# Kernel optimization log

Measured on AMD Instinct MI355X. Metric: run time of the kernel, lower is better.

## Reference

```python
import jax, jax.numpy as jnp
from jax import lax
import numpy as np


def _lap(cost):
    """Jonker-Volgenant shortest-augmenting-path LAP (same optimum as
    scipy.optimize.linear_sum_assignment) on cost [n, m] with n <= m.
    Returns for each row (0..n-1) the assigned column index."""
    n, m = cost.shape
    BIG = jnp.asarray(1e9, cost.dtype)
    a = jnp.pad(cost, ((1, 0), (1, 0)))  # 1-based rows/cols, [n+1, m+1]
    u = jnp.zeros(n + 1, cost.dtype)     # row duals
    v = jnp.zeros(m + 1, cost.dtype)     # col duals
    p = jnp.zeros(m + 1, jnp.int32)      # p[j] = row matched to col j (0 = free)

    def row_step(i, carry):
        u, v, p = carry
        p = p.at[0].set(i)  # virtual col 0 holds the row being inserted
        minv = jnp.full(m + 1, BIG, cost.dtype)
        used = jnp.zeros(m + 1, bool)
        way = jnp.zeros(m + 1, jnp.int32)

        def cond(s):
            u, v, p, way, minv, used, j0 = s
            return p[j0] != 0

        def body(s):
            u, v, p, way, minv, used, j0 = s
            used = used.at[j0].set(True)
            i0 = p[j0]
            cur = a[i0] - u[i0] - v                      # reduced costs, len m+1
            better = (cur < minv) & jnp.logical_not(used)
            minv = jnp.where(better, cur, minv)
            way = jnp.where(better, j0, way)
            masked = jnp.where(used, BIG, minv)
            j1 = jnp.argmin(masked).astype(jnp.int32)
            delta = masked[j1]
            u = u.at[p].add(jnp.where(used, delta, jnp.zeros((), cost.dtype)))
            v = jnp.where(used, v - delta, v)
            minv = jnp.where(used, minv, minv - delta)
            return (u, v, p, way, minv, used, j1)

        u, v, p, way, minv, used, j0 = lax.while_loop(
            cond, body, (u, v, p, way, minv, used, jnp.int32(0)))

        # backtrack the augmenting path
        def cond2(s):
            return s[1] != 0

        def body2(s):
            p, j0 = s
            j1 = way[j0]
            return (p.at[j0].set(p[j1]), j1)

        p, _ = lax.while_loop(cond2, body2, (p, j0))
        return (u, v, p)

    u, v, p = lax.fori_loop(1, n + 1, row_step, (u, v, p))
    # invert: row r (1-based) matched to col j  ->  ans[r-1] = j-1
    cols = jnp.arange(m + 1)
    valid = (p > 0) & (cols > 0)
    idx = jnp.where(valid, p - 1, n)  # invalid entries dumped into scratch slot n
    ans = jnp.zeros(n + 1, jnp.int32).at[idx].set((cols - 1).astype(jnp.int32))
    return ans[:n]


def _cdist_mm(x, y):
    """Batched euclidean cdist via the GEMM trick (torch use_mm_for_euclid_dist)."""
    x2 = jnp.sum(x * x, axis=-1)[..., :, None]   # [B, N, 1]
    y2 = jnp.sum(y * y, axis=-1)[..., None, :]   # [B, 1, M]
    xy = jnp.einsum('bnd,bmd->bnm', x, y)        # [B, N, M]
    return jnp.sqrt(jnp.maximum(x2 + y2 - 2.0 * xy, 0.0))


def setup_inputs() -> dict:
    key = jax.random.key(0)
    k1, k2 = jax.random.split(key)
    outputs = jax.random.normal(k1, (32, 512, 768), dtype=jnp.float32)
    targets = jax.random.normal(k2, (32, 200, 768), dtype=jnp.float32)
    return {"outputs": outputs, "targets": targets}


def reference(outputs, targets):
    # cost[b, n, m] = ||outputs[b, n] - targets[b, m]||_2  (block-diagonal slices
    # of the original cross-batch cdist are all that the matcher consumes)
    cost = _cdist_mm(outputs, targets)                       # [B, N, M]
    # solve with targets as rows (n=M <= m=N): pred column per gt row
    gt_to_pred = jax.vmap(_lap)(jnp.swapaxes(cost, 1, 2))    # [B, M]
    # scipy returns pred indices sorted ascending; replicate that ordering
    order = jnp.argsort(gt_to_pred, axis=1)                  # gt indices (index_j)
    index_i = jnp.take_along_axis(gt_to_pred, order, axis=1)
    index_j = order.astype(jnp.int32)
    return jnp.stack([index_i, index_j], axis=1)             # [B, 2, M] int32
```

## Files before the change

### kernel.cpp

```cpp
#include <hip/hip_runtime.h>
#include <math.h>

static constexpr int BATCH = 32;
static constexpr int NPRED = 512;
static constexpr int NTGT  = 200;
static constexpr int DIM   = 768;
#define BIGF 1e9f
#define INFF __builtin_inff()

__global__ __launch_bounds__(64) void row_norms_kernel(const float* __restrict__ x,
                                                       float* __restrict__ out) {
    int row = blockIdx.x;
    const float4* r = (const float4*)(x + (size_t)row * DIM);
    float s = 0.f;
#pragma unroll
    for (int k = 0; k < 3; ++k) {
        float4 v = r[threadIdx.x + 64 * k];
        s += v.x * v.x + v.y * v.y + v.z * v.z + v.w * v.w;
    }
#pragma unroll
    for (int off = 32; off; off >>= 1) s += __shfl_down(s, off);
    if (threadIdx.x == 0) out[row] = s;
}

__global__ __launch_bounds__(256) void cost_kernel(const float* __restrict__ O,
                                                   const float* __restrict__ T,
                                                   const float* __restrict__ no_arr,
                                                   const float* __restrict__ nt_arr,
                                                   float* __restrict__ cost) {
    const int b  = blockIdx.z;
    const int m0 = blockIdx.y * 64;
    const int n0 = blockIdx.x * 64;
    const float* Tb = T + (size_t)b * NTGT * DIM;
    const float* Ob = O + (size_t)b * NPRED * DIM;

    __shared__ __align__(16) float As[32][68];
    __shared__ __align__(16) float Bs[32][68];

    const int tid = threadIdx.x;
    const int tx = tid & 15;
    const int ty = tid >> 4;

    float acc[4][4] = {};

    for (int k0 = 0; k0 < DIM; k0 += 32) {
#pragma unroll
        for (int q = 0; q < 2; ++q) {
            int f = tid + q * 256;
            int r = f >> 3;
            int kk = (f & 7) << 2;
            int gm = m0 + r; if (gm > NTGT - 1) gm = NTGT - 1;
            float4 vA = *(const float4*)(Tb + (size_t)gm * DIM + k0 + kk);
            As[kk + 0][r] = vA.x; As[kk + 1][r] = vA.y;
            As[kk + 2][r] = vA.z; As[kk + 3][r] = vA.w;
            float4 vB = *(const float4*)(Ob + (size_t)(n0 + r) * DIM + k0 + kk);
            Bs[kk + 0][r] = vB.x; Bs[kk + 1][r] = vB.y;
            Bs[kk + 2][r] = vB.z; Bs[kk + 3][r] = vB.w;
        }
        __syncthreads();
#pragma unroll
        for (int k = 0; k < 32; ++k) {
            float4 a  = *(const float4*)&As[k][ty << 2];
            float4 bv = *(const float4*)&Bs[k][tx << 2];
            acc[0][0] += a.x * bv.x; acc[0][1] += a.x * bv.y;
            acc[0][2] += a.x * bv.z; acc[0][3] += a.x * bv.w;
            acc[1][0] += a.y * bv.x; acc[1][1] += a.y * bv.y;
            acc[1][2] += a.y * bv.z; acc[1][3] += a.y * bv.w;
            acc[2][0] += a.z * bv.x; acc[2][1] += a.z * bv.y;
            acc[2][2] += a.z * bv.z; acc[2][3] += a.z * bv.w;
            acc[3][0] += a.w * bv.x; acc[3][1] += a.w * bv.y;
            acc[3][2] += a.w * bv.z; acc[3][3] += a.w * bv.w;
        }
        __syncthreads();
    }

    {
        float4 nov = *(const float4*)(no_arr + b * NPRED + n0 + (tx << 2));
#pragma unroll
        for (int i = 0; i < 4; ++i) {
            int gm = m0 + (ty << 2) + i;
            if (gm < NTGT) {
                float ntv = nt_arr[b * NTGT + gm];
                float4 o;
                o.x = sqrtf(fmaxf(ntv + nov.x - 2.0f * acc[i][0], 0.0f));
                o.y = sqrtf(fmaxf(ntv + nov.y - 2.0f * acc[i][1], 0.0f));
                o.z = sqrtf(fmaxf(ntv + nov.z - 2.0f * acc[i][2], 0.0f));
                o.w = sqrtf(fmaxf(ntv + nov.w - 2.0f * acc[i][3], 0.0f));
                *(float4*)&cost[((size_t)b * NTGT + gm) * NPRED + n0 + (tx << 2)] = o;
            }
        }
    }
}

__device__ __forceinline__ int rl(int v, int l) {
    return __builtin_amdgcn_readlane(v, l);
}
__device__ __forceinline__ float rlf(float v, int l) {
    return __int_as_float(__builtin_amdgcn_readlane(__float_as_int(v), l));
}
__device__ __forceinline__ int sel8i(const int* a, int s) {
    int r = a[0];
#pragma unroll
    for (int k = 1; k < 8; ++k) r = (s == k) ? a[k] : r;
    return r;
}
__device__ __forceinline__ float sel8f(const float* a, int s) {
    float r = a[0];
#pragma unroll
    for (int k = 1; k < 8; ++k) r = (s == k) ? a[k] : r;
    return r;
}
__device__ __forceinline__ float dpp_min_f32(float x) {
    float t;
    t = __int_as_float(__builtin_amdgcn_update_dpp(__float_as_int(x), __float_as_int(x), 0x111, 0xF, 0xF, false)); x = fminf(x, t);
    t = __int_as_float(__builtin_amdgcn_update_dpp(__float_as_int(x), __float_as_int(x), 0x112, 0xF, 0xF, false)); x = fminf(x, t);
    t = __int_as_float(__builtin_amdgcn_update_dpp(__float_as_int(x), __float_as_int(x), 0x114, 0xF, 0xF, false)); x = fminf(x, t);
    t = __int_as_float(__builtin_amdgcn_update_dpp(__float_as_int(x), __float_as_int(x), 0x118, 0xF, 0xF, false)); x = fminf(x, t);
    t = __int_as_float(__builtin_amdgcn_update_dpp(__float_as_int(x), __float_as_int(x), 0x142, 0xF, 0xF, false)); x = fminf(x, t);
    t = __int_as_float(__builtin_amdgcn_update_dpp(__float_as_int(x), __float_as_int(x), 0x143, 0xF, 0xF, false)); x = fminf(x, t);
    return x;
}
__device__ __forceinline__ float tree8(const float* m, int& lq) {
    float v01 = (m[0] <= m[1]) ? m[0] : m[1];
    int   q01 = (m[0] <= m[1]) ? 0 : 1;
    float v23 = (m[2] <= m[3]) ? m[2] : m[3];
    int   q23 = (m[2] <= m[3]) ? 2 : 3;
    float v45 = (m[4] <= m[5]) ? m[4] : m[5];
    int   q45 = (m[4] <= m[5]) ? 4 : 5;
    float v67 = (m[6] <= m[7]) ? m[6] : m[7];
    int   q67 = (m[6] <= m[7]) ? 6 : 7;
    float v03 = (v01 <= v23) ? v01 : v23;
    int   q03 = (v01 <= v23) ? q01 : q23;
    float v47 = (v45 <= v67) ? v45 : v67;
    int   q47 = (v45 <= v67) ? q45 : q67;
    lq = (v03 <= v47) ? q03 : q47;
    return (v03 <= v47) ? v03 : v47;
}

__global__ __launch_bounds__(64) void lap_kernel(const float* __restrict__ cost,
                                                 int* __restrict__ out) {
    const int b = blockIdx.x;
    const int lane = threadIdx.x;
    const float* C = cost + (size_t)b * NTGT * NPRED;
    const float* Cl = C + lane * 8;

    __shared__ float u0[NTGT + 1];
    __shared__ int g2p[NTGT];

    for (int k = lane; k < NTGT + 1; k += 64) u0[k] = 0.f;

    float v[8], minv[8], up[8];
    int p_arr[8], way_arr[8];
#pragma unroll
    for (int q = 0; q < 8; ++q) {
        v[q] = 0.f; up[q] = 0.f; p_arr[q] = 0; way_arr[q] = 0;
    }
    __syncthreads();

    float4 ca = *(const float4*)(Cl);
    float4 cb = *(const float4*)(Cl + 4);
    float4 sa = ca, sb = cb;

    for (int i = 1; i <= NTGT; ++i) {
#pragma unroll
        for (int q = 0; q < 8; ++q) minv[q] = BIGF;
        float uI = 0.f;
        float u_i0 = 0.f;
        int j0 = 0;
        int j1 = 0;
        int spec_j = 0;

        for (int it = 0; it <= NPRED; ++it) {
            float c[8];
            c[0] = ca.x; c[1] = ca.y; c[2] = ca.z; c[3] = ca.w;
            c[4] = cb.x; c[5] = cb.y; c[6] = cb.z; c[7] = cb.w;

            bool used_b[8];
#pragma unroll
            for (int q = 0; q < 8; ++q) {
                float cur = (c[q] - u_i0) - v[q];
                used_b[q] = (minv[q] == INFF);
                float cure = used_b[q] ? INFF : cur;
                bool imp = cure < minv[q];
                minv[q] = imp ? cure : minv[q];
                way_arr[q] = imp ? j0 : way_arr[q];
            }

            int lq;
            float lval = tree8(minv, lq);
            int   psel = sel8i(p_arr, lq);
            float usel = sel8f(up, lq);
            float wmin = rlf(dpp_min_f32(lval), 63);
            unsigned long long mask = __ballot(lval == wmin);
            int w = (int)__builtin_ctzll(mask);
            int qw  = rl(lq, w);
            int i0n = rl(psel, w);
            float u_n = rlf(usel, w);
            float delta = wmin;
            j1 = w * 8 + qw + 1;
            bool done = (i0n == 0);

            if (!done) {
                if (j1 == spec_j) {
                    ca = sa; cb = sb;
                } else {
                    const float* Crow = Cl + (size_t)(i0n - 1) * NPRED;
                    ca = *(const float4*)(Crow);
                    cb = *(const float4*)(Crow + 4);
                }
                float lv2 = (lane == w) ? INFF : lval;
                float wm2 = rlf(dpp_min_f32(lv2), 63);
                unsigned long long m2 = __ballot(lv2 == wm2);
                int w2 = (int)__builtin_ctzll(m2);
                int q2 = rl(lq, w2);
                int p2 = rl(psel, w2);
                int sj = w2 * 8 + q2 + 1;
                if (p2 != 0 && sj != spec_j) {
                    const float* Srow = Cl + (size_t)(p2 - 1) * NPRED;
                    sa = *(const float4*)(Srow);
                    sb = *(const float4*)(Srow + 4);
                }
                spec_j = sj;
            }

            uI += delta;
#pragma unroll
            for (int q = 0; q < 8; ++q) {
                float d0 = used_b[q] ? delta : 0.f;
                v[q]  -= d0;
                up[q] += d0;
                minv[q] -= delta;
            }
            {
                bool lw = (lane == w);
#pragma unroll
                for (int q = 0; q < 8; ++q)
                    minv[q] = (lw && q == qw) ? INFF : minv[q];
            }

            if (done) break;
            u_i0 = u_n;
            j0 = j1;
        }

        if (i < NTGT) {
            const float* Crow = Cl + (size_t)i * NPRED;
            ca = *(const float4*)(Crow);
            cb = *(const float4*)(Crow + 4);
        }

#pragma unroll
        for (int q = 0; q < 8; ++q) {
            bool usedq = (minv[q] == INFF);
            if (usedq && p_arr[q] != 0) u0[p_arr[q]] = up[q];
        }
        if (lane == 0) u0[i] = uI;

        {
            int j = j1;
            for (int s = 0; s <= NPRED; ++s) {
                int ow = (j - 1) >> 3, oq = (j - 1) & 7;
                int wj = rl(sel8i(way_arr, oq), ow);
                int pOfW;
                if (wj == 0) {
                    pOfW = i;
                } else {
                    int ow2 = (wj - 1) >> 3, oq2 = (wj - 1) & 7;
                    pOfW = rl(sel8i(p_arr, oq2), ow2);
                }
#pragma unroll
                for (int q = 0; q < 8; ++q) {
                    bool mine = (lane == ow) && (q == oq);
                    p_arr[q] = mine ? pOfW : p_arr[q];
                }
                if (wj == 0) break;
                j = wj;
            }
        }

        __syncthreads();
#pragma unroll
        for (int q = 0; q < 8; ++q) up[q] = u0[p_arr[q]];
    }

#pragma unroll
    for (int q = 0; q < 8; ++q) {
        int r = p_arr[q];
        if (r > 0) g2p[r - 1] = lane * 8 + q;
    }
    __syncthreads();

    for (int t = lane; t < NTGT; t += 64) {
        int myv = g2p[t];
        int rank = 0;
        for (int l = 0; l < NTGT; ++l) rank += (g2p[l] < myv) ? 1 : 0;
        out[b * 2 * NTGT + rank] = myv;
        out[b * 2 * NTGT + NTGT + rank] = t;
    }
}

extern "C" void kernel_launch(void* const* d_in, const int* in_sizes, int n_in,
                              void* d_out, int out_size, void* d_ws, size_t ws_size,
                              hipStream_t stream) {
    const float* outputs = (const float*)d_in[0];
    const float* targets = (const float*)d_in[1];
    int* out = (int*)d_out;

    float* cost   = (float*)d_ws;
    float* no_arr = cost + (size_t)BATCH * NTGT * NPRED;
    float* nt_arr = no_arr + (size_t)BATCH * NPRED;

    row_norms_kernel<<<BATCH * NPRED, 64, 0, stream>>>(outputs, no_arr);
    row_norms_kernel<<<BATCH * NTGT, 64, 0, stream>>>(targets, nt_arr);
    cost_kernel<<<dim3(NPRED / 64, (NTGT + 63) / 64, BATCH), 256, 0, stream>>>(
        outputs, targets, no_arr, nt_arr, cost);
    lap_kernel<<<BATCH, 64, 0, stream>>>(cost, out);
}
```

Measured before the change: 790.7 us.

## Merge norm kernels, enlarge cost GEMM tile, use NaN as the LAP used-marker

Merges the two row-norm launches into a single kernel and doubles the cost GEMM tile along the target dimension (128 rows, 8x4 accumulators per thread), cutting launches and improving data reuse. In the LAP inner loop, used columns are now marked with quiet NaN instead of infinity. Because comparisons against NaN are false and fminf ignores NaN, the per-column masking select drops out and the 8-way argmin becomes an fminf tree. The LAP dominates runtime, so the NaN trick in its serial loop matters most. The larger tile reduces the grid to 2 row-blocks, where the last block is mostly padding, and raises register pressure.

```diff
diff --git a/kernel.cpp b/kernel.cpp
--- a/kernel.cpp
+++ b/kernel.cpp
@@ -6,12 +6,22 @@
 static constexpr int NTGT  = 200;
 static constexpr int DIM   = 768;
 #define BIGF 1e9f
-#define INFF __builtin_inff()
-
-__global__ __launch_bounds__(64) void row_norms_kernel(const float* __restrict__ x,
-                                                       float* __restrict__ out) {
+#define QNANF __int_as_float(0x7fc00000)
+
+__global__ __launch_bounds__(64) void norms_kernel(const float* __restrict__ O,
+                                                   const float* __restrict__ T,
+                                                   float* __restrict__ no_arr,
+                                                   float* __restrict__ nt_arr) {
     int row = blockIdx.x;
-    const float4* r = (const float4*)(x + (size_t)row * DIM);
+    const float* src;
+    float* dst;
+    if (row < BATCH * NPRED) {
+        src = O + (size_t)row * DIM;            dst = no_arr + row;
+    } else {
+        int r2 = row - BATCH * NPRED;
+        src = T + (size_t)r2 * DIM;             dst = nt_arr + r2;
+    }
+    const float4* r = (const float4*)src;
     float s = 0.f;
 #pragma unroll
     for (int k = 0; k < 3; ++k) {
@@ -20,7 +30,7 @@
     }
 #pragma unroll
     for (int off = 32; off; off >>= 1) s += __shfl_down(s, off);
-    if (threadIdx.x == 0) out[row] = s;
+    if (threadIdx.x == 0) *dst = s;
 }
 
 __global__ __launch_bounds__(256) void cost_kernel(const float* __restrict__ O,
@@ -29,23 +39,23 @@
                                                    const float* __restrict__ nt_arr,
                                                    float* __restrict__ cost) {
     const int b  = blockIdx.z;
-    const int m0 = blockIdx.y * 64;
+    const int m0 = blockIdx.y * 128;
     const int n0 = blockIdx.x * 64;
     const float* Tb = T + (size_t)b * NTGT * DIM;
     const float* Ob = O + (size_t)b * NPRED * DIM;
 
-    __shared__ __align__(16) float As[32][68];
+    __shared__ __align__(16) float As[32][132];
     __shared__ __align__(16) float Bs[32][68];
 
     const int tid = threadIdx.x;
     const int tx = tid & 15;
     const int ty = tid >> 4;
 
-    float acc[4][4] = {};
+    float acc[8][4] = {};
 
     for (int k0 = 0; k0 < DIM; k0 += 32) {
 #pragma unroll
-        for (int q = 0; q < 2; ++q) {
+        for (int q = 0; q < 4; ++q) {
             int f = tid + q * 256;
             int r = f >> 3;
             int kk = (f & 7) << 2;
@@ -53,6 +63,12 @@
             float4 vA = *(const float4*)(Tb + (size_t)gm * DIM + k0 + kk);
             As[kk + 0][r] = vA.x; As[kk + 1][r] = vA.y;
             As[kk + 2][r] = vA.z; As[kk + 3][r] = vA.w;
+        }
+#pragma unroll
+        for (int q = 0; q < 2; ++q) {
+            int f = tid + q * 256;
+            int r = f >> 3;
+            int kk = (f & 7) << 2;
             float4 vB = *(const float4*)(Ob + (size_t)(n0 + r) * DIM + k0 + kk);
             Bs[kk + 0][r] = vB.x; Bs[kk + 1][r] = vB.y;
             Bs[kk + 2][r] = vB.z; Bs[kk + 3][r] = vB.w;
@@ -60,16 +76,15 @@
         __syncthreads();
 #pragma unroll
         for (int k = 0; k < 32; ++k) {
-            float4 a  = *(const float4*)&As[k][ty << 2];
-            float4 bv = *(const float4*)&Bs[k][tx << 2];
-            acc[0][0] += a.x * bv.x; acc[0][1] += a.x * bv.y;
-            acc[0][2] += a.x * bv.z; acc[0][3] += a.x * bv.w;
-            acc[1][0] += a.y * bv.x; acc[1][1] += a.y * bv.y;
-            acc[1][2] += a.y * bv.z; acc[1][3] += a.y * bv.w;
-            acc[2][0] += a.z * bv.x; acc[2][1] += a.z * bv.y;
-            acc[2][2] += a.z * bv.z; acc[2][3] += a.z * bv.w;
-            acc[3][0] += a.w * bv.x; acc[3][1] += a.w * bv.y;
-            acc[3][2] += a.w * bv.z; acc[3][3] += a.w * bv.w;
+            float4 a0 = *(const float4*)&As[k][ty * 8];
+            float4 a1 = *(const float4*)&As[k][ty * 8 + 4];
+            float4 bv = *(const float4*)&Bs[k][tx * 4];
+            float av[8] = {a0.x, a0.y, a0.z, a0.w, a1.x, a1.y, a1.z, a1.w};
+#pragma unroll
+            for (int i = 0; i < 8; ++i) {
+                acc[i][0] += av[i] * bv.x; acc[i][1] += av[i] * bv.y;
+                acc[i][2] += av[i] * bv.z; acc[i][3] += av[i] * bv.w;
+            }
         }
         __syncthreads();
     }
@@ -77,8 +92,8 @@
     {
         float4 nov = *(const float4*)(no_arr + b * NPRED + n0 + (tx << 2));
 #pragma unroll
-        for (int i = 0; i < 4; ++i) {
-            int gm = m0 + (ty << 2) + i;
+        for (int i = 0; i < 8; ++i) {
+            int gm = m0 + ty * 8 + i;
             if (gm < NTGT) {
                 float ntv = nt_arr[b * NTGT + gm];
                 float4 o;
@@ -120,21 +135,15 @@
     t = __int_as_float(__builtin_amdgcn_update_dpp(__float_as_int(x), __float_as_int(x), 0x143, 0xF, 0xF, false)); x = fminf(x, t);
     return x;
 }
-__device__ __forceinline__ float tree8(const float* m, int& lq) {
-    float v01 = (m[0] <= m[1]) ? m[0] : m[1];
-    int   q01 = (m[0] <= m[1]) ? 0 : 1;
-    float v23 = (m[2] <= m[3]) ? m[2] : m[3];
-    int   q23 = (m[2] <= m[3]) ? 2 : 3;
-    float v45 = (m[4] <= m[5]) ? m[4] : m[5];
-    int   q45 = (m[4] <= m[5]) ? 4 : 5;
-    float v67 = (m[6] <= m[7]) ? m[6] : m[7];
-    int   q67 = (m[6] <= m[7]) ? 6 : 7;
-    float v03 = (v01 <= v23) ? v01 : v23;
-    int   q03 = (v01 <= v23) ? q01 : q23;
-    float v47 = (v45 <= v67) ? v45 : v67;
-    int   q47 = (v45 <= v67) ? q45 : q67;
-    lq = (v03 <= v47) ? q03 : q47;
-    return (v03 <= v47) ? v03 : v47;
+__device__ __forceinline__ float tree8n(const float* m, int& lq) {
+    float v01 = fminf(m[0], m[1]); int q01 = (v01 == m[0]) ? 0 : 1;
+    float v23 = fminf(m[2], m[3]); int q23 = (v23 == m[2]) ? 2 : 3;
+    float v45 = fminf(m[4], m[5]); int q45 = (v45 == m[4]) ? 4 : 5;
+    float v67 = fminf(m[6], m[7]); int q67 = (v67 == m[6]) ? 6 : 7;
+    float v03 = fminf(v01, v23);   int q03 = (v03 == v01) ? q01 : q23;
+    float v47 = fminf(v45, v67);   int q47 = (v47 == v45) ? q45 : q67;
+    float r = fminf(v03, v47);     lq = (r == v03) ? q03 : q47;
+    return r;
 }
 
 __global__ __launch_bounds__(64) void lap_kernel(const float* __restrict__ cost,
@@ -178,16 +187,15 @@
             bool used_b[8];
 #pragma unroll
             for (int q = 0; q < 8; ++q) {
+                used_b[q] = __builtin_isnan(minv[q]);
                 float cur = (c[q] - u_i0) - v[q];
-                used_b[q] = (minv[q] == INFF);
-                float cure = used_b[q] ? INFF : cur;
-                bool imp = cure < minv[q];
-                minv[q] = imp ? cure : minv[q];
+                bool imp = cur < minv[q];
+                minv[q] = imp ? cur : minv[q];
                 way_arr[q] = imp ? j0 : way_arr[q];
             }
 
             int lq;
-            float lval = tree8(minv, lq);
+            float lval = tree8n(minv, lq);
             int   psel = sel8i(p_arr, lq);
             float usel = sel8f(up, lq);
             float wmin = rlf(dpp_min_f32(lval), 63);
@@ -208,7 +216,7 @@
                     ca = *(const float4*)(Crow);
                     cb = *(const float4*)(Crow + 4);
                 }
-                float lv2 = (lane == w) ? INFF : lval;
+                float lv2 = (lane == w) ? QNANF : lval;
                 float wm2 = rlf(dpp_min_f32(lv2), 63);
                 unsigned long long m2 = __ballot(lv2 == wm2);
                 int w2 = (int)__builtin_ctzll(m2);
@@ -235,7 +243,7 @@
                 bool lw = (lane == w);
 #pragma unroll
                 for (int q = 0; q < 8; ++q)
-                    minv[q] = (lw && q == qw) ? INFF : minv[q];
+                    minv[q] = (lw && q == qw) ? QNANF : minv[q];
             }
 
             if (done) break;
@@ -251,7 +259,7 @@
 
 #pragma unroll
         for (int q = 0; q < 8; ++q) {
-            bool usedq = (minv[q] == INFF);
+            bool usedq = __builtin_isnan(minv[q]);
             if (usedq && p_arr[q] != 0) u0[p_arr[q]] = up[q];
         }
         if (lane == 0) u0[i] = uI;
@@ -310,9 +318,9 @@
     float* no_arr = cost + (size_t)BATCH * NTGT * NPRED;
     float* nt_arr = no_arr + (size_t)BATCH * NPRED;
 
-    row_norms_kernel<<<BATCH * NPRED, 64, 0, stream>>>(outputs, no_arr);
-    row_norms_kernel<<<BATCH * NTGT, 64, 0, stream>>>(targets, nt_arr);
-    cost_kernel<<<dim3(NPRED / 64, (NTGT + 63) / 64, BATCH), 256, 0, stream>>>(
+    norms_kernel<<<BATCH * (NPRED + NTGT), 64, 0, stream>>>(outputs, targets,
+                                                            no_arr, nt_arr);
+    cost_kernel<<<dim3(NPRED / 64, (NTGT + 127) / 128, BATCH), 256, 0, stream>>>(
         outputs, targets, no_arr, nt_arr, cost);
     lap_kernel<<<BATCH, 64, 0, stream>>>(cost, out);
 }
```

Measured after the change: 766.9 us. 3.0% less time.
